# Kernel optimization log

Hardware: AMD Instinct MI355X
Metric: run time of the kernel (lower is better)

Reference implementation:

```python
import jax, jax.numpy as jnp
import numpy as np

N = 512
D = 400          # per-sample feature dim (lstm_hidden_dim * 2)
H = 400          # hidden dim of F_func (lstm_hidden_dim * 2)


def setup_inputs() -> dict:
    key = jax.random.key(0)
    k1, k2, k3, k4, k5, k6 = jax.random.split(key, 6)
    x_samples = jax.random.normal(k1, (N, D), dtype=jnp.float32)
    y_samples = jax.random.normal(k2, (N, D), dtype=jnp.float32)
    # torch nn.Linear default init: U(-1/sqrt(fan_in), 1/sqrt(fan_in))
    b1_bound = 1.0 / np.sqrt(2 * D)
    b2_bound = 1.0 / np.sqrt(H)
    W1 = jax.random.uniform(k3, (H, 2 * D), minval=-b1_bound, maxval=b1_bound, dtype=jnp.float32)
    b1 = jax.random.uniform(k4, (H,), minval=-b1_bound, maxval=b1_bound, dtype=jnp.float32)
    W2 = jax.random.uniform(k5, (1, H), minval=-b2_bound, maxval=b2_bound, dtype=jnp.float32)
    b2 = jax.random.uniform(k6, (1,), minval=-b2_bound, maxval=b2_bound, dtype=jnp.float32)
    return {"x_samples": x_samples, "y_samples": y_samples,
            "W1": W1, "b1": b1, "W2": W2, "b2": b2}


def reference(x_samples, y_samples, W1, b1, W2, b2):
    n = y_samples.shape[0]
    W1x, W1y = W1[:, :D], W1[:, D:]
    hx = x_samples @ W1x.T          # [N, H], contribution of x
    hy = y_samples @ W1y.T          # [N, H], contribution of y

    def score(h):  # second linear + softplus, squeeze out last dim of 1
        return jax.nn.softplus(h @ W2.T + b2)[..., 0]

    # T0[i] = F(x[i], y[i])
    T0 = score(jax.nn.relu(hx + hy + b1))                      # [N]
    # T1[i, j] = F(x[j], y[i])  (x tiled along dim 0, y along dim 1)
    h_pair = jax.nn.relu(hy[:, None, :] + hx[None, :, :] + b1) # [N, N, H]
    T1 = score(h_pair)                                          # [N, N]

    t0_mean = T0.mean()
    lower_bound = t0_mean - (jax.nn.logsumexp(T1, axis=1).mean() - jnp.log(jnp.float32(n)))
    upper_bound = t0_mean - T1.mean()
    return (lower_bound, upper_bound)
```

## Files before the change

kernel.cpp:

```cpp
#include <hip/hip_runtime.h>
#include <math.h>


#define NSAMP 512
#define DIM 400
#define HID 400

__global__ __launch_bounds__(256) void club_gemm_kernel(
    const float* __restrict__ X, const float* __restrict__ Y,
    const float* __restrict__ W1, const float* __restrict__ b1,
    float* __restrict__ hxT0, float* __restrict__ hxT1,
    float* __restrict__ hyb0, float* __restrict__ hyb1)
{
    __shared__ __align__(16) float Ls[64 * 204];
    const int t    = threadIdx.x;
    const int lane = t & 63;
    const int wave = __builtin_amdgcn_readfirstlane(t >> 6);
    const int b    = blockIdx.x;

    const float* __restrict__ Lbase;
    const float* __restrict__ Sbase;
    int Lstride, Lcol0, Lrow0, Lrowmax, Sstride, Scol0, srow_base;
    int kh, mat;

    if (b < 400) {
        mat = 0; kh = b & 1;
        const int bx = (b >> 1) & 7, by = b >> 4;
        Lbase = X;  Lstride = DIM;     Lcol0 = 0;   Lrow0 = bx * 64; Lrowmax = NSAMP - 1;
        Sbase = W1; Sstride = 2 * DIM; Scol0 = 0;
        srow_base = by * 16 + wave * 4;
    } else {
        mat = 1;
        const int bb = b - 400; kh = bb & 1;
        const int bx = (bb >> 1) & 31, by = bb >> 6;
        Lbase = W1; Lstride = 2 * DIM; Lcol0 = DIM; Lrow0 = by * 64; Lrowmax = HID - 1;
        Sbase = Y;  Sstride = DIM;     Scol0 = 0;
        srow_base = bx * 16 + wave * 4;
    }
    const int kc0 = kh * 200;

    for (int idx = t; idx < 3200; idx += 256) {
        int row = idx / 50, q = idx % 50;
        int r = Lrow0 + row; if (r > Lrowmax) r = Lrowmax;
        float4 v = *(const float4*)(Lbase + (size_t)r * Lstride + Lcol0 + kc0 + 4 * q);
        *(float4*)(Ls + row * 204 + 4 * q) = v;
    }
    __syncthreads();

    float acc[4] = {0.f, 0.f, 0.f, 0.f};
#pragma unroll 2
    for (int k4 = 0; k4 < 50; k4++) {
        float4 xv = *(const float4*)(Ls + lane * 204 + 4 * k4);
#pragma unroll
        for (int c = 0; c < 4; c++) {
            const float* __restrict__ wp =
                Sbase + (size_t)(srow_base + c) * Sstride + Scol0 + kc0 + 4 * k4;
            float4 wv = *(const float4*)wp;
            acc[c] = fmaf(xv.x, wv.x, acc[c]);
            acc[c] = fmaf(xv.y, wv.y, acc[c]);
            acc[c] = fmaf(xv.z, wv.z, acc[c]);
            acc[c] = fmaf(xv.w, wv.w, acc[c]);
        }
    }

    if (mat == 0) {
        float* __restrict__ dst = kh ? hxT1 : hxT0;
#pragma unroll
        for (int c = 0; c < 4; c++)
            dst[(size_t)(srow_base + c) * NSAMP + Lrow0 + lane] = acc[c];
    } else {
        float* __restrict__ dst = kh ? hyb1 : hyb0;
        const int h = Lrow0 + lane;
        if (h < HID) {
            if (kh == 0) {
                float bv = b1[h];
#pragma unroll
                for (int c = 0; c < 4; c++) acc[c] += bv;
            }
#pragma unroll
            for (int c = 0; c < 4; c++)
                dst[(size_t)(srow_base + c) * HID + h] = acc[c];
        }
    }
}

__global__ __launch_bounds__(256) void club_combine_kernel(
    const float4* __restrict__ hxT0, const float4* __restrict__ hxT1,
    const float4* __restrict__ hyb0, const float4* __restrict__ hyb1,
    float4* __restrict__ hxT, float4* __restrict__ hyb)
{
    const int idx = blockIdx.x * 256 + threadIdx.x;
    if (idx < 51200) {
        float4 a = hxT0[idx], b = hxT1[idx];
        hxT[idx] = make_float4(a.x + b.x, a.y + b.y, a.z + b.z, a.w + b.w);
    } else {
        const int k = idx - 51200;
        float4 a = hyb0[k], b = hyb1[k];
        hyb[k] = make_float4(a.x + b.x, a.y + b.y, a.z + b.z, a.w + b.w);
    }
}

__global__ __launch_bounds__(256) void club_pair_kernel(
    const float* __restrict__ hxT, const float* __restrict__ hyb,
    const float* __restrict__ W2, const float* __restrict__ b2,
    double* __restrict__ expsum, double* __restrict__ tsum,
    double* __restrict__ diagT)
{
    const int t    = threadIdx.x;
    const int lane = t & 63;
    const int wave = __builtin_amdgcn_readfirstlane(t >> 6);
    const int jx   = blockIdx.x;
    const int j    = jx * 64 + lane;
    const int i    = blockIdx.y * 4 + wave;

    const float* __restrict__ Bp = hxT + j;
    const float* __restrict__ Ap = hyb + (size_t)i * HID;

    float acc0 = 0.f, acc1 = 0.f;
#pragma unroll 2
    for (int g = 0; g < 50; g++) {
        const int h = 8 * g;
        float bv[8];
#pragma unroll
        for (int u = 0; u < 8; u++)
            bv[u] = Bp[(size_t)(h + u) * NSAMP];
        float4 a0 = *(const float4*)(Ap + h);
        float4 a1 = *(const float4*)(Ap + h + 4);
        float4 w0 = *(const float4*)(W2 + h);
        float4 w1 = *(const float4*)(W2 + h + 4);
        acc0 = fmaf(fmaxf(a0.x + bv[0], 0.f), w0.x, acc0);
        acc1 = fmaf(fmaxf(a0.y + bv[1], 0.f), w0.y, acc1);
        acc0 = fmaf(fmaxf(a0.z + bv[2], 0.f), w0.z, acc0);
        acc1 = fmaf(fmaxf(a0.w + bv[3], 0.f), w0.w, acc1);
        acc0 = fmaf(fmaxf(a1.x + bv[4], 0.f), w1.x, acc0);
        acc1 = fmaf(fmaxf(a1.y + bv[5], 0.f), w1.y, acc1);
        acc0 = fmaf(fmaxf(a1.z + bv[6], 0.f), w1.z, acc0);
        acc1 = fmaf(fmaxf(a1.w + bv[7], 0.f), w1.w, acc1);
    }

    float s  = (acc0 + acc1) + b2[0];
    float es = expf(s);
    float T  = log1pf(es);
    if (j == i) diagT[i] = (double)T;
    double eD = 1.0 + (double)es;
    double tD = (double)T;
    for (int off = 32; off > 0; off >>= 1) {
        eD += __shfl_down(eD, off);
        tD += __shfl_down(tD, off);
    }
    if (lane == 0) {
        expsum[i * 8 + jx] = eD;
        tsum  [i * 8 + jx] = tD;
    }
}

__global__ __launch_bounds__(512) void club_final_kernel(
    const double* __restrict__ expsum, const double* __restrict__ tsum,
    const double* __restrict__ diagT, float* __restrict__ out)
{
    __shared__ double sh[3 * 512];
    const int t = threadIdx.x;
    double es = 0.0, ts = 0.0;
#pragma unroll
    for (int b = 0; b < 8; b++) { es += expsum[t * 8 + b]; ts += tsum[t * 8 + b]; }
    sh[t] = log(es); sh[512 + t] = ts; sh[1024 + t] = diagT[t];
    __syncthreads();
    for (int off = 256; off > 0; off >>= 1) {
        if (t < off) {
            sh[t]        += sh[t + off];
            sh[512 + t]  += sh[512 + t + off];
            sh[1024 + t] += sh[1024 + t + off];
        }
        __syncthreads();
    }
    if (t == 0) {
        double t0m  = sh[1024] / 512.0;
        double lsem = sh[0]    / 512.0;
        double t1m  = sh[512]  / (512.0 * 512.0);
        out[0] = (float)(t0m - (lsem - log(512.0)));
        out[1] = (float)(t0m - t1m);
    }
}

extern "C" void kernel_launch(void* const* d_in, const int* in_sizes, int n_in,
                              void* d_out, int out_size, void* d_ws, size_t ws_size,
                              hipStream_t stream) {
    const float* X  = (const float*)d_in[0];
    const float* Y  = (const float*)d_in[1];
    const float* W1 = (const float*)d_in[2];
    const float* b1 = (const float*)d_in[3];
    const float* W2 = (const float*)d_in[4];
    const float* b2 = (const float*)d_in[5];
    float* out = (float*)d_out;

    char* ws = (char*)d_ws;
    float*  hxT0   = (float*) (ws);
    float*  hxT1   = (float*) (ws +  819200);
    float*  hyb0   = (float*) (ws + 1638400);
    float*  hyb1   = (float*) (ws + 2457600);
    float*  hxT    = (float*) (ws + 3276800);
    float*  hyb    = (float*) (ws + 4096000);
    double* expsum = (double*)(ws + 4915200);
    double* tsum   = (double*)(ws + 4947968);
    double* diagT  = (double*)(ws + 4980736);

    club_gemm_kernel   <<<dim3(848),    256, 0, stream>>>(X, Y, W1, b1,
                                                          hxT0, hxT1, hyb0, hyb1);
    club_combine_kernel<<<dim3(400),    256, 0, stream>>>((const float4*)hxT0, (const float4*)hxT1,
                                                          (const float4*)hyb0, (const float4*)hyb1,
                                                          (float4*)hxT, (float4*)hyb);
    club_pair_kernel   <<<dim3(8, 128), 256, 0, stream>>>(hxT, hyb, W2, b2,
                                                          expsum, tsum, diagT);
    club_final_kernel  <<<1, 512, 0, stream>>>(expsum, tsum, diagT, out);
}
```

Baseline: 109.6 us.

## Drop split-K GEMM with combine kernel; compute two rows per wave in pair kernel

The GEMM kernel now loops over both K halves inside one block instead of splitting K across blocks. This removes the partial-sum buffers and the separate combine kernel launch, at the cost of halving the GEMM grid to 424 blocks. The pair kernel now has each wave handle two i rows, so each hxT column load is reused twice and the grid height is halved. This cuts global load traffic per output but lowers parallelism and raises register use.

```diff
diff --git a/kernel.cpp b/kernel.cpp
--- a/kernel.cpp
+++ b/kernel.cpp
@@ -9,8 +9,7 @@
 __global__ __launch_bounds__(256) void club_gemm_kernel(
     const float* __restrict__ X, const float* __restrict__ Y,
     const float* __restrict__ W1, const float* __restrict__ b1,
-    float* __restrict__ hxT0, float* __restrict__ hxT1,
-    float* __restrict__ hyb0, float* __restrict__ hyb1)
+    float* __restrict__ hxT, float* __restrict__ hyb)
 {
     __shared__ __align__(16) float Ls[64 * 204];
     const int t    = threadIdx.x;
@@ -20,83 +19,67 @@
 
     const float* __restrict__ Lbase;
     const float* __restrict__ Sbase;
-    int Lstride, Lcol0, Lrow0, Lrowmax, Sstride, Scol0, srow_base;
-    int kh, mat;
-
-    if (b < 400) {
-        mat = 0; kh = b & 1;
-        const int bx = (b >> 1) & 7, by = b >> 4;
+    int Lstride, Lcol0, Lrow0, Lrowmax, Sstride, srow_base;
+    int mat;
+
+    if (b < 200) {
+        mat = 0;
+        const int bx = b & 7, by = b >> 3;
         Lbase = X;  Lstride = DIM;     Lcol0 = 0;   Lrow0 = bx * 64; Lrowmax = NSAMP - 1;
-        Sbase = W1; Sstride = 2 * DIM; Scol0 = 0;
+        Sbase = W1; Sstride = 2 * DIM;
         srow_base = by * 16 + wave * 4;
     } else {
         mat = 1;
-        const int bb = b - 400; kh = bb & 1;
-        const int bx = (bb >> 1) & 31, by = bb >> 6;
+        const int bb = b - 200;
+        const int bx = bb & 31, by = bb >> 5;
         Lbase = W1; Lstride = 2 * DIM; Lcol0 = DIM; Lrow0 = by * 64; Lrowmax = HID - 1;
-        Sbase = Y;  Sstride = DIM;     Scol0 = 0;
+        Sbase = Y;  Sstride = DIM;
         srow_base = bx * 16 + wave * 4;
     }
-    const int kc0 = kh * 200;
-
-    for (int idx = t; idx < 3200; idx += 256) {
-        int row = idx / 50, q = idx % 50;
-        int r = Lrow0 + row; if (r > Lrowmax) r = Lrowmax;
-        float4 v = *(const float4*)(Lbase + (size_t)r * Lstride + Lcol0 + kc0 + 4 * q);
-        *(float4*)(Ls + row * 204 + 4 * q) = v;
-    }
-    __syncthreads();
 
     float acc[4] = {0.f, 0.f, 0.f, 0.f};
+
+#pragma unroll 1
+    for (int half = 0; half < 2; half++) {
+        const int kc0 = half * 200;
+        if (half) __syncthreads();
+
+        for (int idx = t; idx < 3200; idx += 256) {
+            int row = idx / 50, q = idx % 50;
+            int r = Lrow0 + row; if (r > Lrowmax) r = Lrowmax;
+            float4 v = *(const float4*)(Lbase + (size_t)r * Lstride + Lcol0 + kc0 + 4 * q);
+            *(float4*)(Ls + row * 204 + 4 * q) = v;
+        }
+        __syncthreads();
+
 #pragma unroll 2
-    for (int k4 = 0; k4 < 50; k4++) {
-        float4 xv = *(const float4*)(Ls + lane * 204 + 4 * k4);
-#pragma unroll
-        for (int c = 0; c < 4; c++) {
-            const float* __restrict__ wp =
-                Sbase + (size_t)(srow_base + c) * Sstride + Scol0 + kc0 + 4 * k4;
-            float4 wv = *(const float4*)wp;
-            acc[c] = fmaf(xv.x, wv.x, acc[c]);
-            acc[c] = fmaf(xv.y, wv.y, acc[c]);
-            acc[c] = fmaf(xv.z, wv.z, acc[c]);
-            acc[c] = fmaf(xv.w, wv.w, acc[c]);
+        for (int k4 = 0; k4 < 50; k4++) {
+            float4 xv = *(const float4*)(Ls + lane * 204 + 4 * k4);
+#pragma unroll
+            for (int c = 0; c < 4; c++) {
+                const float* __restrict__ wp =
+                    Sbase + (size_t)(srow_base + c) * Sstride + kc0 + 4 * k4;
+                float4 wv = *(const float4*)wp;
+                acc[c] = fmaf(xv.x, wv.x, acc[c]);
+                acc[c] = fmaf(xv.y, wv.y, acc[c]);
+                acc[c] = fmaf(xv.z, wv.z, acc[c]);
+                acc[c] = fmaf(xv.w, wv.w, acc[c]);
+            }
         }
     }
 
     if (mat == 0) {
-        float* __restrict__ dst = kh ? hxT1 : hxT0;
 #pragma unroll
         for (int c = 0; c < 4; c++)
-            dst[(size_t)(srow_base + c) * NSAMP + Lrow0 + lane] = acc[c];
+            hxT[(size_t)(srow_base + c) * NSAMP + Lrow0 + lane] = acc[c];
     } else {
-        float* __restrict__ dst = kh ? hyb1 : hyb0;
         const int h = Lrow0 + lane;
         if (h < HID) {
-            if (kh == 0) {
-                float bv = b1[h];
-#pragma unroll
-                for (int c = 0; c < 4; c++) acc[c] += bv;
-            }
+            const float bv = b1[h];
 #pragma unroll
             for (int c = 0; c < 4; c++)
-                dst[(size_t)(srow_base + c) * HID + h] = acc[c];
-        }
-    }
-}
-
-__global__ __launch_bounds__(256) void club_combine_kernel(
-    const float4* __restrict__ hxT0, const float4* __restrict__ hxT1,
-    const float4* __restrict__ hyb0, const float4* __restrict__ hyb1,
-    float4* __restrict__ hxT, float4* __restrict__ hyb)
-{
-    const int idx = blockIdx.x * 256 + threadIdx.x;
-    if (idx < 51200) {
-        float4 a = hxT0[idx], b = hxT1[idx];
-        hxT[idx] = make_float4(a.x + b.x, a.y + b.y, a.z + b.z, a.w + b.w);
-    } else {
-        const int k = idx - 51200;
-        float4 a = hyb0[k], b = hyb1[k];
-        hyb[k] = make_float4(a.x + b.x, a.y + b.y, a.z + b.z, a.w + b.w);
+                hyb[(size_t)(srow_base + c) * HID + h] = acc[c] + bv;
+        }
     }
 }
 
@@ -111,12 +94,15 @@
     const int wave = __builtin_amdgcn_readfirstlane(t >> 6);
     const int jx   = blockIdx.x;
     const int j    = jx * 64 + lane;
-    const int i    = blockIdx.y * 4 + wave;
-
-    const float* __restrict__ Bp = hxT + j;
-    const float* __restrict__ Ap = hyb + (size_t)i * HID;
-
-    float acc0 = 0.f, acc1 = 0.f;
+    const int i0   = blockIdx.y * 8 + wave * 2;
+    const int i1   = i0 + 1;
+
+    const float* __restrict__ Bp  = hxT + j;
+    const float* __restrict__ Ap0 = hyb + (size_t)i0 * HID;
+    const float* __restrict__ Ap1 = hyb + (size_t)i1 * HID;
+
+    float a0s = 0.f, a1s = 0.f;
+    float b0s = 0.f, b1s = 0.f;
 #pragma unroll 2
     for (int g = 0; g < 50; g++) {
         const int h = 8 * g;
@@ -124,33 +110,51 @@
 #pragma unroll
         for (int u = 0; u < 8; u++)
             bv[u] = Bp[(size_t)(h + u) * NSAMP];
-        float4 a0 = *(const float4*)(Ap + h);
-        float4 a1 = *(const float4*)(Ap + h + 4);
+        float4 p0 = *(const float4*)(Ap0 + h);
+        float4 p1 = *(const float4*)(Ap0 + h + 4);
+        float4 q0 = *(const float4*)(Ap1 + h);
+        float4 q1 = *(const float4*)(Ap1 + h + 4);
         float4 w0 = *(const float4*)(W2 + h);
         float4 w1 = *(const float4*)(W2 + h + 4);
-        acc0 = fmaf(fmaxf(a0.x + bv[0], 0.f), w0.x, acc0);
-        acc1 = fmaf(fmaxf(a0.y + bv[1], 0.f), w0.y, acc1);
-        acc0 = fmaf(fmaxf(a0.z + bv[2], 0.f), w0.z, acc0);
-        acc1 = fmaf(fmaxf(a0.w + bv[3], 0.f), w0.w, acc1);
-        acc0 = fmaf(fmaxf(a1.x + bv[4], 0.f), w1.x, acc0);
-        acc1 = fmaf(fmaxf(a1.y + bv[5], 0.f), w1.y, acc1);
-        acc0 = fmaf(fmaxf(a1.z + bv[6], 0.f), w1.z, acc0);
-        acc1 = fmaf(fmaxf(a1.w + bv[7], 0.f), w1.w, acc1);
-    }
-
-    float s  = (acc0 + acc1) + b2[0];
-    float es = expf(s);
-    float T  = log1pf(es);
-    if (j == i) diagT[i] = (double)T;
-    double eD = 1.0 + (double)es;
-    double tD = (double)T;
+        a0s = fmaf(fmaxf(p0.x + bv[0], 0.f), w0.x, a0s);
+        a1s = fmaf(fmaxf(p0.y + bv[1], 0.f), w0.y, a1s);
+        a0s = fmaf(fmaxf(p0.z + bv[2], 0.f), w0.z, a0s);
+        a1s = fmaf(fmaxf(p0.w + bv[3], 0.f), w0.w, a1s);
+        a0s = fmaf(fmaxf(p1.x + bv[4], 0.f), w1.x, a0s);
+        a1s = fmaf(fmaxf(p1.y + bv[5], 0.f), w1.y, a1s);
+        a0s = fmaf(fmaxf(p1.z + bv[6], 0.f), w1.z, a0s);
+        a1s = fmaf(fmaxf(p1.w + bv[7], 0.f), w1.w, a1s);
+        b0s = fmaf(fmaxf(q0.x + bv[0], 0.f), w0.x, b0s);
+        b1s = fmaf(fmaxf(q0.y + bv[1], 0.f), w0.y, b1s);
+        b0s = fmaf(fmaxf(q0.z + bv[2], 0.f), w0.z, b0s);
+        b1s = fmaf(fmaxf(q0.w + bv[3], 0.f), w0.w, b1s);
+        b0s = fmaf(fmaxf(q1.x + bv[4], 0.f), w1.x, b0s);
+        b1s = fmaf(fmaxf(q1.y + bv[5], 0.f), w1.y, b1s);
+        b0s = fmaf(fmaxf(q1.z + bv[6], 0.f), w1.z, b0s);
+        b1s = fmaf(fmaxf(q1.w + bv[7], 0.f), w1.w, b1s);
+    }
+
+    const float bias = b2[0];
+    float s0  = (a0s + a1s) + bias;
+    float s1  = (b0s + b1s) + bias;
+    float es0 = expf(s0), es1 = expf(s1);
+    float T0  = log1pf(es0);
+    float T1  = log1pf(es1);
+    if (j == i0) diagT[i0] = (double)T0;
+    if (j == i1) diagT[i1] = (double)T1;
+    double e0 = 1.0 + (double)es0, t0 = (double)T0;
+    double e1 = 1.0 + (double)es1, t1 = (double)T1;
     for (int off = 32; off > 0; off >>= 1) {
-        eD += __shfl_down(eD, off);
-        tD += __shfl_down(tD, off);
+        e0 += __shfl_down(e0, off);
+        t0 += __shfl_down(t0, off);
+        e1 += __shfl_down(e1, off);
+        t1 += __shfl_down(t1, off);
     }
     if (lane == 0) {
-        expsum[i * 8 + jx] = eD;
-        tsum  [i * 8 + jx] = tD;
+        expsum[i0 * 8 + jx] = e0;
+        tsum  [i0 * 8 + jx] = t0;
+        expsum[i1 * 8 + jx] = e1;
+        tsum  [i1 * 8 + jx] = t1;
     }
 }
 
@@ -194,22 +198,14 @@
     float* out = (float*)d_out;
 
     char* ws = (char*)d_ws;
-    float*  hxT0   = (float*) (ws);
-    float*  hxT1   = (float*) (ws +  819200);
-    float*  hyb0   = (float*) (ws + 1638400);
-    float*  hyb1   = (float*) (ws + 2457600);
-    float*  hxT    = (float*) (ws + 3276800);
-    float*  hyb    = (float*) (ws + 4096000);
-    double* expsum = (double*)(ws + 4915200);
-    double* tsum   = (double*)(ws + 4947968);
-    double* diagT  = (double*)(ws + 4980736);
-
-    club_gemm_kernel   <<<dim3(848),    256, 0, stream>>>(X, Y, W1, b1,
-                                                          hxT0, hxT1, hyb0, hyb1);
-    club_combine_kernel<<<dim3(400),    256, 0, stream>>>((const float4*)hxT0, (const float4*)hxT1,
-                                                          (const float4*)hyb0, (const float4*)hyb1,
-                                                          (float4*)hxT, (float4*)hyb);
-    club_pair_kernel   <<<dim3(8, 128), 256, 0, stream>>>(hxT, hyb, W2, b2,
-                                                          expsum, tsum, diagT);
-    club_final_kernel  <<<1, 512, 0, stream>>>(expsum, tsum, diagT, out);
-}
+    float*  hxT    = (float*) (ws);
+    float*  hyb    = (float*) (ws +  819200);
+    double* expsum = (double*)(ws + 1638400);
+    double* tsum   = (double*)(ws + 1671168);
+    double* diagT  = (double*)(ws + 1703936);
+
+    club_gemm_kernel <<<dim3(424),    256, 0, stream>>>(X, Y, W1, b1, hxT, hyb);
+    club_pair_kernel <<<dim3(8, 64),  256, 0, stream>>>(hxT, hyb, W2, b2,
+                                                        expsum, tsum, diagT);
+    club_final_kernel<<<1, 512, 0, stream>>>(expsum, tsum, diagT, out);
+}
```

Result: no change. 109.7 us (+0.1%).
